# Kernel tuning notes

Measured on AMD Instinct MI355X. Metric: run time of the kernel, lower is better.

The kernel has to match this reference:

```python
import jax, jax.numpy as jnp
import numpy as np

NUM_CATEGORIES = 64
IN_DIM = 1024
OUT_DIM = 1024
BATCH = 32
SEQ = 512


def setup_inputs() -> dict:
    key = jax.random.key(0)
    k1, k2, k3 = jax.random.split(key, 3)
    x = jax.random.normal(k1, (BATCH, SEQ, IN_DIM), dtype=jnp.float32)
    category_ids = jax.random.randint(k2, (BATCH,), 0, NUM_CATEGORIES, dtype=jnp.int32)
    weight = (jax.random.normal(k3, (NUM_CATEGORIES, IN_DIM, OUT_DIM), dtype=jnp.float32) * 0.02)
    bias = jnp.zeros((NUM_CATEGORIES, OUT_DIM), dtype=jnp.float32)
    return {"x": x, "category_ids": category_ids, "weight": weight, "bias": bias}


def reference(x, category_ids, weight, bias):
    # Gather per-sample weights/biases: W [b, in, out], b [b, out]
    W = weight[category_ids]
    b = bias[category_ids]
    # x: [b, l, in] -> out: [b, l, out]
    return jnp.einsum('bli,bio->blo', x, W) + b[:, None, :]
```

## Files before the change

kernel.cpp:

```cpp
#include <hip/hip_runtime.h>

#define NUM_CATEGORIES 64
#define IN_DIM 1024
#define OUT_DIM 1024
#define BATCH 32
#define SEQ 512

#define BM 256
#define BN 256
#define BK 64
#define NSTEP (IN_DIM / BK)

#define LDA 72
#define LDBW 260

typedef float f32x4 __attribute__((ext_vector_type(4)));
typedef unsigned int u32x2 __attribute__((ext_vector_type(2)));
typedef unsigned int u32x4 __attribute__((ext_vector_type(4)));
typedef __bf16 bf16x8 __attribute__((ext_vector_type(8)));

__device__ inline unsigned int f2bf_rne(float f) {
    unsigned int u = __builtin_bit_cast(unsigned int, f);
    return (u + 0x7FFFu + ((u >> 16) & 1u)) >> 16;
}
__device__ inline unsigned int pack2(float lo, float hi) {
    return f2bf_rne(lo) | (f2bf_rne(hi) << 16);
}

__global__ __launch_bounds__(512, 2)
void cslinear_kernel(const float* __restrict__ x,
                     const int* __restrict__ cid,
                     const float* __restrict__ weight,
                     const float* __restrict__ bias,
                     float* __restrict__ out) {
    __shared__ unsigned short As[2][BM * LDA];
    __shared__ unsigned int   Bs[2][(BK / 2) * LDBW];

    const int t    = threadIdx.x;
    const int lane = t & 63;
    const int w    = t >> 6;

    const int s    = blockIdx.x;
    const int xcd  = s & 7;
    const int ixd  = s >> 3;
    const int b    = xcd + 8 * (ixd >> 3);
    const int j    = ixd & 7;
    const int nt   = j & 3;
    const int mt   = j >> 2;

    const int c = cid[b];
    const float* Wp = weight + (size_t)c * IN_DIM * OUT_DIM + (size_t)nt * BN;
    const float* Xp = x + ((size_t)b * SEQ + (size_t)mt * BM) * IN_DIM;
    float* Op = out + ((size_t)b * SEQ + (size_t)mt * BM) * OUT_DIM + (size_t)nt * BN;

    f32x4 acc[8][4] = {};

    const int mbase = (w >> 2) * 128;
    const int nbase = (w & 3) * 64;
    const int lrow  = lane & 15;
    const int lhi   = lane >> 4;

    f32x4 ra[8];
    f32x4 rb0[4], rb1[4];

    auto LOADT = [&](int ks) {
        const float* Xk = Xp + ks * BK;
        #pragma unroll
        for (int i = 0; i < 8; ++i) {
            int f   = i * 512 + t;
            int row = f >> 4;
            int c4  = f & 15;
            ra[i] = *reinterpret_cast<const f32x4*>(Xk + (size_t)row * IN_DIM + c4 * 4);
        }
        const float* Wk = Wp + (size_t)(ks * BK) * OUT_DIM;
        #pragma unroll
        for (int i = 0; i < 4; ++i) {
            int u  = i * 512 + t;
            int kp = u >> 6;
            int n4 = u & 63;
            const float* bse = Wk + (size_t)(2 * kp) * OUT_DIM + n4 * 4;
            rb0[i] = *reinterpret_cast<const f32x4*>(bse);
            rb1[i] = *reinterpret_cast<const f32x4*>(bse + OUT_DIM);
        }
    };

    auto STORET = [&](int p) {
        char* AsB = reinterpret_cast<char*>(&As[p][0]);
        #pragma unroll
        for (int i = 0; i < 8; ++i) {
            int f   = i * 512 + t;
            int row = f >> 4;
            int c4  = f & 15;
            u32x2 q;
            q.x = pack2(ra[i].x, ra[i].y);
            q.y = pack2(ra[i].z, ra[i].w);
            *reinterpret_cast<u32x2*>(AsB + row * (LDA * 2) + c4 * 8) = q;
        }
        unsigned int* BsW = &Bs[p][0];
        #pragma unroll
        for (int i = 0; i < 4; ++i) {
            int u  = i * 512 + t;
            int kp = u >> 6;
            int n4 = u & 63;
            u32x4 q;
            #pragma unroll
            for (int jj = 0; jj < 4; ++jj)
                q[jj] = pack2(rb0[i][jj], rb1[i][jj]);
            *reinterpret_cast<u32x4*>(BsW + kp * LDBW + n4 * 4) = q;
        }
    };

    LOADT(0);

    for (int ks = 0; ks < NSTEP; ++ks) {
        const int p = ks & 1;

        STORET(p);
        if (ks + 1 < NSTEP) LOADT(ks + 1);

        asm volatile("s_waitcnt lgkmcnt(0)" ::: "memory");
        __builtin_amdgcn_s_barrier();
        __builtin_amdgcn_sched_barrier(0);

        const char* AsB = reinterpret_cast<const char*>(&As[p][0]);
        const unsigned int* BsW = &Bs[p][0];

        #pragma unroll
        for (int kk = 0; kk < 2; ++kk) {
            bf16x8 bfr[4];
            #pragma unroll
            for (int ni = 0; ni < 4; ++ni) {
                int n   = nbase + ni * 16 + lrow;
                int kp0 = kk * 16 + lhi * 4;
                u32x4 wds;
                #pragma unroll
                for (int jj = 0; jj < 4; ++jj)
                    wds[jj] = BsW[(kp0 + jj) * LDBW + n];
                bfr[ni] = __builtin_bit_cast(bf16x8, wds);
            }
            #pragma unroll
            for (int mi = 0; mi < 8; ++mi) {
                int r = mbase + mi * 16 + lrow;
                bf16x8 afr = *reinterpret_cast<const bf16x8*>(
                    AsB + r * (LDA * 2) + kk * 64 + lhi * 16);
                #pragma unroll
                for (int ni = 0; ni < 4; ++ni)
                    acc[mi][ni] = __builtin_amdgcn_mfma_f32_16x16x32_bf16(
                        afr, bfr[ni], acc[mi][ni], 0, 0, 0);
            }
        }
    }

    const int lcol  = lane & 15;
    const int lrow4 = (lane >> 4) * 4;
    float bv[4];
    #pragma unroll
    for (int ni = 0; ni < 4; ++ni)
        bv[ni] = bias[(size_t)c * OUT_DIM + nt * BN + nbase + ni * 16 + lcol];

    #pragma unroll
    for (int mi = 0; mi < 8; ++mi) {
        int rbase = mbase + mi * 16 + lrow4;
        #pragma unroll
        for (int ni = 0; ni < 4; ++ni) {
            int ncol = nbase + ni * 16 + lcol;
            #pragma unroll
            for (int r = 0; r < 4; ++r) {
                Op[(size_t)(rbase + r) * OUT_DIM + ncol] = acc[mi][ni][r] + bv[ni];
            }
        }
    }
}

extern "C" void kernel_launch(void* const* d_in, const int* in_sizes, int n_in,
                              void* d_out, int out_size, void* d_ws, size_t ws_size,
                              hipStream_t stream) {
    const float* x      = (const float*)d_in[0];
    const int*   cid    = (const int*)d_in[1];
    const float* weight = (const float*)d_in[2];
    const float* bias   = (const float*)d_in[3];
    float* out = (float*)d_out;

    dim3 grid(256);
    dim3 block(512);
    hipLaunchKernelGGL(cslinear_kernel, grid, block, 0, stream,
                       x, cid, weight, bias, out);
}
```

Baseline: 60.24 us.

## Interleave LDS stores and global loads with MFMA quadrants in a ping-pong schedule

Restructures the K loop into four sub-phases per tile. Each phase issues LDS reads for the next MFMA quadrant, a slice of the bf16 stores for the next buffer, and the split A/B global loads, separated by barriers, and the MFMA blocks are raised in priority with s_setprio. The fp32-to-bf16 conversion uses the compiler's vector convert in place of manual rounding. The aim is to hide LDS write and global load latency behind MFMA work, at the cost of four extra barriers per K tile.

```diff
diff --git a/kernel.cpp b/kernel.cpp
--- a/kernel.cpp
+++ b/kernel.cpp
@@ -1,4 +1,5 @@
 #include <hip/hip_runtime.h>
+#include <type_traits>
 
 #define NUM_CATEGORIES 64
 #define IN_DIM 1024
@@ -9,23 +10,17 @@
 #define BM 256
 #define BN 256
 #define BK 64
-#define NSTEP (IN_DIM / BK)
+#define NT (IN_DIM / BK)
 
 #define LDA 72
 #define LDBW 260
 
 typedef float f32x4 __attribute__((ext_vector_type(4)));
-typedef unsigned int u32x2 __attribute__((ext_vector_type(2)));
+typedef float f32x2 __attribute__((ext_vector_type(2)));
 typedef unsigned int u32x4 __attribute__((ext_vector_type(4)));
+typedef __bf16 bf16x2 __attribute__((ext_vector_type(2)));
+typedef __bf16 bf16x4 __attribute__((ext_vector_type(4)));
 typedef __bf16 bf16x8 __attribute__((ext_vector_type(8)));
-
-__device__ inline unsigned int f2bf_rne(float f) {
-    unsigned int u = __builtin_bit_cast(unsigned int, f);
-    return (u + 0x7FFFu + ((u >> 16) & 1u)) >> 16;
-}
-__device__ inline unsigned int pack2(float lo, float hi) {
-    return f2bf_rne(lo) | (f2bf_rne(hi) << 16);
-}
 
 __global__ __launch_bounds__(512, 2)
 void cslinear_kernel(const float* __restrict__ x,
@@ -63,7 +58,7 @@
     f32x4 ra[8];
     f32x4 rb0[4], rb1[4];
 
-    auto LOADT = [&](int ks) {
+    auto LOAD_A = [&](int ks) {
         const float* Xk = Xp + ks * BK;
         #pragma unroll
         for (int i = 0; i < 8; ++i) {
@@ -72,6 +67,8 @@
             int c4  = f & 15;
             ra[i] = *reinterpret_cast<const f32x4*>(Xk + (size_t)row * IN_DIM + c4 * 4);
         }
+    };
+    auto LOAD_B = [&](int ks) {
         const float* Wk = Wp + (size_t)(ks * BK) * OUT_DIM;
         #pragma unroll
         for (int i = 0; i < 4; ++i) {
@@ -84,72 +81,130 @@
         }
     };
 
-    auto STORET = [&](int p) {
-        char* AsB = reinterpret_cast<char*>(&As[p][0]);
-        #pragma unroll
-        for (int i = 0; i < 8; ++i) {
-            int f   = i * 512 + t;
-            int row = f >> 4;
-            int c4  = f & 15;
-            u32x2 q;
-            q.x = pack2(ra[i].x, ra[i].y);
-            q.y = pack2(ra[i].z, ra[i].w);
-            *reinterpret_cast<u32x2*>(AsB + row * (LDA * 2) + c4 * 8) = q;
-        }
-        unsigned int* BsW = &Bs[p][0];
-        #pragma unroll
-        for (int i = 0; i < 4; ++i) {
-            int u  = i * 512 + t;
-            int kp = u >> 6;
-            int n4 = u & 63;
-            u32x4 q;
+    auto ST_A1 = [&](unsigned short* Abuf, int i) {
+        char* AsB = reinterpret_cast<char*>(Abuf);
+        int f   = i * 512 + t;
+        int row = f >> 4;
+        int c4  = f & 15;
+        bf16x4 a4 = __builtin_convertvector(ra[i], bf16x4);
+        *reinterpret_cast<bf16x4*>(AsB + row * (LDA * 2) + c4 * 8) = a4;
+    };
+    auto ST_B1 = [&](unsigned int* Bbuf, int i) {
+        int u  = i * 512 + t;
+        int kp = u >> 6;
+        int n4 = u & 63;
+        u32x4 q;
+        #pragma unroll
+        for (int jj = 0; jj < 4; ++jj) {
+            f32x2 pr;
+            pr.x = rb0[i][jj];
+            pr.y = rb1[i][jj];
+            bf16x2 pb = __builtin_convertvector(pr, bf16x2);
+            q[jj] = __builtin_bit_cast(unsigned int, pb);
+        }
+        *reinterpret_cast<u32x4*>(Bbuf + kp * LDBW + n4 * 4) = q;
+    };
+
+    auto RD_B = [&](const unsigned int* Bbuf, int kk, bf16x8* bfr) {
+        #pragma unroll
+        for (int ni = 0; ni < 4; ++ni) {
+            int n   = nbase + ni * 16 + lrow;
+            int kp0 = kk * 16 + lhi * 4;
+            u32x4 wds;
             #pragma unroll
             for (int jj = 0; jj < 4; ++jj)
-                q[jj] = pack2(rb0[i][jj], rb1[i][jj]);
-            *reinterpret_cast<u32x4*>(BsW + kp * LDBW + n4 * 4) = q;
-        }
-    };
-
-    LOADT(0);
-
-    for (int ks = 0; ks < NSTEP; ++ks) {
-        const int p = ks & 1;
-
-        STORET(p);
-        if (ks + 1 < NSTEP) LOADT(ks + 1);
-
+                wds[jj] = Bbuf[(kp0 + jj) * LDBW + n];
+            bfr[ni] = __builtin_bit_cast(bf16x8, wds);
+        }
+    };
+    auto RD_A = [&](const unsigned short* Abuf, int mih, int kk, bf16x8* afr) {
+        const char* AsB = reinterpret_cast<const char*>(Abuf);
+        #pragma unroll
+        for (int m2 = 0; m2 < 4; ++m2) {
+            int r = mbase + (mih * 4 + m2) * 16 + lrow;
+            afr[m2] = *reinterpret_cast<const bf16x8*>(AsB + r * (LDA * 2) + kk * 64 + lhi * 16);
+        }
+    };
+    auto QUAD = [&](auto MIH, const bf16x8* afr, const bf16x8* bfr) {
+        constexpr int mih = decltype(MIH)::value;
+        __builtin_amdgcn_s_setprio(1);
+        #pragma unroll
+        for (int m2 = 0; m2 < 4; ++m2) {
+            #pragma unroll
+            for (int ni = 0; ni < 4; ++ni)
+                acc[mih * 4 + m2][ni] = __builtin_amdgcn_mfma_f32_16x16x32_bf16(
+                    afr[m2], bfr[ni], acc[mih * 4 + m2][ni], 0, 0, 0);
+        }
+        __builtin_amdgcn_s_setprio(0);
+    };
+
+    constexpr std::integral_constant<int, 0> M0{};
+    constexpr std::integral_constant<int, 1> M1{};
+    constexpr std::integral_constant<int, 0> S0{};
+    constexpr std::integral_constant<int, 1> S1{};
+
+    auto FENCE = [&]() {
+        __builtin_amdgcn_s_barrier();
         asm volatile("s_waitcnt lgkmcnt(0)" ::: "memory");
-        __builtin_amdgcn_s_barrier();
         __builtin_amdgcn_sched_barrier(0);
-
-        const char* AsB = reinterpret_cast<const char*>(&As[p][0]);
-        const unsigned int* BsW = &Bs[p][0];
-
-        #pragma unroll
-        for (int kk = 0; kk < 2; ++kk) {
-            bf16x8 bfr[4];
-            #pragma unroll
-            for (int ni = 0; ni < 4; ++ni) {
-                int n   = nbase + ni * 16 + lrow;
-                int kp0 = kk * 16 + lhi * 4;
-                u32x4 wds;
-                #pragma unroll
-                for (int jj = 0; jj < 4; ++jj)
-                    wds[jj] = BsW[(kp0 + jj) * LDBW + n];
-                bfr[ni] = __builtin_bit_cast(bf16x8, wds);
-            }
-            #pragma unroll
-            for (int mi = 0; mi < 8; ++mi) {
-                int r = mbase + mi * 16 + lrow;
-                bf16x8 afr = *reinterpret_cast<const bf16x8*>(
-                    AsB + r * (LDA * 2) + kk * 64 + lhi * 16);
-                #pragma unroll
-                for (int ni = 0; ni < 4; ++ni)
-                    acc[mi][ni] = __builtin_amdgcn_mfma_f32_16x16x32_bf16(
-                        afr, bfr[ni], acc[mi][ni], 0, 0, 0);
-            }
-        }
+    };
+
+    auto KTILE = [&](auto Sr, auto DoStore, auto DoLoad, int tload) {
+        constexpr int sr = decltype(Sr)::value;
+        constexpr bool do_store = decltype(DoStore)::value;
+        constexpr bool do_load  = decltype(DoLoad)::value;
+        const unsigned short* Ab = &As[sr][0];
+        const unsigned int*   Bb = &Bs[sr][0];
+        unsigned short* Aw = &As[sr ^ 1][0];
+        unsigned int*   Bw = &Bs[sr ^ 1][0];
+        bf16x8 bfr[4], afr[4];
+
+        RD_B(Bb, 0, bfr);
+        RD_A(Ab, 0, 0, afr);
+        if (do_store) { ST_A1(Aw, 0); ST_A1(Aw, 1); ST_A1(Aw, 2); ST_A1(Aw, 3); }
+        FENCE();
+        QUAD(M0, afr, bfr);
+        __builtin_amdgcn_s_barrier();
+
+        RD_A(Ab, 1, 0, afr);
+        if (do_store) { ST_A1(Aw, 4); ST_A1(Aw, 5); ST_A1(Aw, 6); ST_A1(Aw, 7); }
+        if (do_load)  LOAD_A(tload);
+        FENCE();
+        QUAD(M1, afr, bfr);
+        __builtin_amdgcn_s_barrier();
+
+        RD_B(Bb, 1, bfr);
+        RD_A(Ab, 0, 1, afr);
+        if (do_store) { ST_B1(Bw, 0); ST_B1(Bw, 1); }
+        FENCE();
+        QUAD(M0, afr, bfr);
+        __builtin_amdgcn_s_barrier();
+
+        RD_A(Ab, 1, 1, afr);
+        if (do_store) { ST_B1(Bw, 2); ST_B1(Bw, 3); }
+        if (do_load)  LOAD_B(tload);
+        FENCE();
+        QUAD(M1, afr, bfr);
+        __builtin_amdgcn_s_barrier();
+    };
+
+    constexpr std::integral_constant<bool, true>  T{};
+    constexpr std::integral_constant<bool, false> F{};
+
+    LOAD_A(0); LOAD_B(0);
+    ST_A1(&As[0][0], 0); ST_A1(&As[0][0], 1); ST_A1(&As[0][0], 2); ST_A1(&As[0][0], 3);
+    ST_A1(&As[0][0], 4); ST_A1(&As[0][0], 5); ST_A1(&As[0][0], 6); ST_A1(&As[0][0], 7);
+    ST_B1(&Bs[0][0], 0); ST_B1(&Bs[0][0], 1); ST_B1(&Bs[0][0], 2); ST_B1(&Bs[0][0], 3);
+    LOAD_A(1); LOAD_B(1);
+    asm volatile("s_waitcnt lgkmcnt(0)" ::: "memory");
+    __builtin_amdgcn_s_barrier();
+
+    for (int tt = 0; tt < NT - 2; tt += 2) {
+        KTILE(S0, T, T, tt + 2);
+        KTILE(S1, T, T, tt + 3);
     }
+    KTILE(S0, T, F, 0);
+    KTILE(S1, F, F, 0);
 
     const int lcol  = lane & 15;
     const int lrow4 = (lane >> 4) * 4;
```

New measurement: 165.3 us. 2.74x slower.
